# Kernel tuning notes

Measured on AMD Instinct MI355X. Metric: run time of the kernel, lower is better.

## Reference

```python
import math
import jax, jax.numpy as jnp
import numpy as np

B, T, D, H = 4, 1024, 1024, 8
HD = D // H  # head_dim = 128

def _trigram_dirs():
    # 8 trigrams = all sign combinations in {−1,+1}^3, L2-normalized (p=2, dim=1)
    t = np.array([[(i >> b & 1) * 2 - 1 for b in (2, 1, 0)] for i in range(8)], dtype=np.float32)
    return jnp.asarray(t / np.linalg.norm(t, axis=1, keepdims=True))

def setup_inputs() -> dict:
    key = jax.random.key(0)
    k1, k2, k3, k4 = jax.random.split(key, 4)
    x = jax.random.normal(k1, (B, T, D), dtype=jnp.float32)
    Wqkv = jax.random.normal(k2, (D, 3 * D), dtype=jnp.float32) * 0.02
    Wout = jax.random.normal(k3, (D, D), dtype=jnp.float32) * 0.02
    # head_scales init to 0 in the module; use nonzero values so the geo-bias path is exercised
    head_scales = jax.random.normal(k4, (H,), dtype=jnp.float32) * 0.1
    head_dirs = _trigram_dirs()  # [H, 3] buffer
    return {"x": x, "Wqkv": Wqkv, "Wout": Wout, "head_scales": head_scales, "head_dirs": head_dirs}

def reference(x, Wqkv, Wout, head_scales, head_dirs):
    b, t, d = x.shape
    scale = 1.0 / math.sqrt(HD)
    qkv = (x @ Wqkv).reshape(b, t, 3, H, HD)
    qkv = jnp.transpose(qkv, (2, 0, 3, 1, 4))  # [3, B, H, T, HD]
    q, k, v = qkv[0], qkv[1], qkv[2]
    # scores: [B, H, T, T]
    scores = jnp.einsum('bhqd,bhkd->bhqk', q, k) * scale
    # rank-1 trigram geometric bias from first 3 dims of q/k
    q_proj = jnp.einsum('bhtd,hd->bht', q[..., :3], head_dirs)
    k_proj = jnp.einsum('bhtd,hd->bht', k[..., :3], head_dirs)
    geo_bias = q_proj[..., :, None] * k_proj[..., None, :]  # [B, H, T, T]
    scores = scores + head_scales[None, :, None, None] * geo_bias
    causal = jnp.tril(jnp.ones((t, t), dtype=bool))
    scores = jnp.where(causal, scores, -jnp.inf)
    attn = jax.nn.softmax(scores, axis=-1)
    out = jnp.einsum('bhqk,bhkd->bhqd', attn, v)  # [B, H, T, HD]
    out = jnp.transpose(out, (0, 2, 1, 3)).reshape(b, t, d)
    return out @ Wout
```

## Files before the change

kernel.cpp:

```cpp
#include <hip/hip_runtime.h>
#include <stdint.h>

typedef __attribute__((ext_vector_type(8))) short short8;
typedef __attribute__((ext_vector_type(4))) short short4v;
typedef __attribute__((ext_vector_type(4))) float f32x4;

__device__ __forceinline__ short f2bf(float x) {
  union { float f; uint32_t u; } c; c.f = x;
  uint32_t r = (c.u + 0x7FFFu + ((c.u >> 16) & 1u)) >> 16;
  return (short)r;
}
__device__ __forceinline__ float b2f(short s) {
  union { uint32_t u; float f; } c; c.u = ((uint32_t)(uint16_t)s) << 16;
  return c.f;
}

__global__ __launch_bounds__(256) void cvt_kernel(const float* __restrict__ in,
                                                  short* __restrict__ out, int n4) {
  int i = blockIdx.x * 256 + threadIdx.x;
  const int stride = gridDim.x * 256;
  for (; i < n4; i += stride) {
    float4 v = reinterpret_cast<const float4*>(in)[i];
    short4v o;
    o.x = f2bf(v.x); o.y = f2bf(v.y); o.z = f2bf(v.z); o.w = f2bf(v.w);
    reinterpret_cast<short4v*>(out)[i] = o;
  }
}

__global__ __launch_bounds__(256) void tcvt_kernel(const float* __restrict__ in,
                                                   short* __restrict__ out, int K, int N) {
  __shared__ __align__(16) short tile[32][33];
  const int nb = blockIdx.x * 32, kb = blockIdx.y * 32;
  const int tx = threadIdx.x & 31, ty = threadIdx.x >> 5;
#pragma unroll
  for (int i = 0; i < 32; i += 8)
    tile[ty + i][tx] = f2bf(in[(size_t)(kb + ty + i) * N + nb + tx]);
  __syncthreads();
#pragma unroll
  for (int i = 0; i < 32; i += 8)
    out[(size_t)(nb + ty + i) * K + kb + tx] = tile[tx][ty + i];
}

__global__ __launch_bounds__(256) void vtrans_kernel(const short* __restrict__ qkvb,
                                                     short* __restrict__ vT) {
  __shared__ __align__(16) short tile[64][65];
  const int b = blockIdx.z;
  const int kv0 = blockIdx.x * 64, c0 = blockIdx.y * 64;
  const int tx = threadIdx.x & 15, ty = threadIdx.x >> 4;
  const short* src = qkvb + (size_t)(b * 1024) * 3072 + 2048;
#pragma unroll
  for (int i = 0; i < 64; i += 16) {
    int r = ty + i;
#pragma unroll
    for (int j = 0; j < 4; ++j)
      tile[r][tx * 4 + j] = src[(size_t)(kv0 + r) * 3072 + c0 + tx * 4 + j];
  }
  __syncthreads();
  short* dst = vT + (size_t)b * 1024 * 1024;
#pragma unroll
  for (int i = 0; i < 64; i += 16) {
    int cc = ty + i;
#pragma unroll
    for (int j = 0; j < 4; ++j)
      dst[(size_t)(c0 + cc) * 1024 + kv0 + tx * 4 + j] = tile[tx * 4 + j][cc];
  }
}

__global__ __launch_bounds__(256) void kproj_kernel(const short* __restrict__ qkvb,
                                                    const float* __restrict__ hdirs,
                                                    float* __restrict__ kproj) {
  const int i = blockIdx.x * 256 + threadIdx.x;
  const int bh = i >> 10, tt = i & 1023;
  const int b = bh >> 3, h = bh & 7;
  const float d0 = hdirs[h * 3], d1 = hdirs[h * 3 + 1], d2 = hdirs[h * 3 + 2];
  const short* kr = qkvb + (size_t)(b * 1024 + tt) * 3072 + 1024 + h * 128;
  kproj[i] = b2f(kr[0]) * d0 + b2f(kr[1]) * d1 + b2f(kr[2]) * d2;
}

template <int OUT_BF16>
__global__ __launch_bounds__(256) void gemm_kernel(const short* __restrict__ A,
                                                   const short* __restrict__ Bt,
                                                   void* __restrict__ Cout,
                                                   int K, int ldc) {
  __shared__ __align__(16) short Al[2][128 * 32];
  __shared__ __align__(16) short Bl[2][128 * 32];
  const int t = threadIdx.x;
  const int lane = t & 63, w = t >> 6;
  const int wr = w >> 1, wc = w & 1;
  const int g = lane >> 4, c16 = lane & 15;
  const int row0 = blockIdx.y * 128, col0 = blockIdx.x * 128;

  f32x4 acc[4][4];
#pragma unroll
  for (int m = 0; m < 4; ++m)
#pragma unroll
    for (int n = 0; n < 4; ++n) {
      f32x4 z = {0.0f, 0.0f, 0.0f, 0.0f};
      acc[m][n] = z;
    }

  auto stage = [&](int buf, int kt) {
    const int k0 = kt * 32;
#pragma unroll
    for (int i = 0; i < 2; ++i) {
      const int qb = i * 256 + (t & 192);
      const int q = qb + lane;
      const int r = q >> 2;
      const int c = (q & 3) ^ ((r >> 1) & 3);
      const short* ga = A + (size_t)(row0 + r) * K + k0 + c * 8;
      const short* gb = Bt + (size_t)(col0 + r) * K + k0 + c * 8;
      __builtin_amdgcn_global_load_lds((const __attribute__((address_space(1))) void*)ga,
                                       (__attribute__((address_space(3))) void*)&Al[buf][qb * 8],
                                       16, 0, 0);
      __builtin_amdgcn_global_load_lds((const __attribute__((address_space(1))) void*)gb,
                                       (__attribute__((address_space(3))) void*)&Bl[buf][qb * 8],
                                       16, 0, 0);
    }
  };

  stage(0, 0);
  __syncthreads();
  const int NK = K >> 5;
  int cur = 0;
  const int rA0 = wr * 64 + c16;
  const int rB0 = wc * 64 + c16;
  for (int kt = 0; kt < NK; ++kt) {
    if (kt + 1 < NK) stage(cur ^ 1, kt + 1);
    short8 aF[4], bF[4];
#pragma unroll
    for (int m = 0; m < 4; ++m) {
      const int r = rA0 + m * 16;
      const int c = g ^ ((r >> 1) & 3);
      aF[m] = *reinterpret_cast<const short8*>(&Al[cur][r * 32 + c * 8]);
    }
#pragma unroll
    for (int n = 0; n < 4; ++n) {
      const int r = rB0 + n * 16;
      const int c = g ^ ((r >> 1) & 3);
      bF[n] = *reinterpret_cast<const short8*>(&Bl[cur][r * 32 + c * 8]);
    }
#pragma unroll
    for (int m = 0; m < 4; ++m)
#pragma unroll
      for (int n = 0; n < 4; ++n)
        acc[m][n] = __builtin_amdgcn_mfma_f32_16x16x32_bf16(aF[m], bF[n], acc[m][n], 0, 0, 0);
    __syncthreads();
    cur ^= 1;
  }

  const int er = row0 + wr * 64 + g * 4;
  const int ec = col0 + wc * 64 + c16;
#pragma unroll
  for (int m = 0; m < 4; ++m)
#pragma unroll
    for (int n = 0; n < 4; ++n)
#pragma unroll
      for (int j = 0; j < 4; ++j) {
        const size_t off = (size_t)(er + m * 16 + j) * ldc + ec + n * 16;
        if (OUT_BF16)
          ((short*)Cout)[off] = f2bf(acc[m][n][j]);
        else
          ((float*)Cout)[off] = acc[m][n][j];
      }
}

__global__ __launch_bounds__(256) void attn_kernel(const short* __restrict__ qkvb,
                                                   const short* __restrict__ vT,
                                                   const float* __restrict__ head_scales,
                                                   const float* __restrict__ hdirs,
                                                   const float* __restrict__ kproj,
                                                   short* __restrict__ attnb) {
  __shared__ __align__(16) short Kl[2][64 * 128];
  __shared__ __align__(16) short Vl[2][128 * 64];
  __shared__ __align__(16) short P_lds[4][16 * 64];

  const int bid = blockIdx.x;
  const int bh = (bid & 7) * 4 + ((bid >> 3) & 3);
  const int qt = 15 - (bid >> 5);
  const int b = bh >> 3, h = bh & 7;
  const int t = threadIdx.x, lane = t & 63, w = t >> 6;
  const int g = lane >> 4, c16 = lane & 15;
  const int q0w = qt * 64 + w * 16;

  const short* qbase = qkvb + (size_t)(b * 1024) * 3072 + h * 128;
  const short* kbase = qbase + 1024;
  const short* vtb = vT + (size_t)bh * 128 * 1024;
  const float* kp = kproj + bh * 1024;

  const float hs = head_scales[h];
  const float d0 = hdirs[h * 3], d1 = hdirs[h * 3 + 1], d2 = hdirs[h * 3 + 2];
  const float scale = 0.08838834764831845f;

  short8 aQ[4];
  float hqp[4];
  {
    const short* qr = qbase + (size_t)(q0w + c16) * 3072 + g * 8;
#pragma unroll
    for (int kk = 0; kk < 4; ++kk) aQ[kk] = *reinterpret_cast<const short8*>(qr + kk * 32);
#pragma unroll
    for (int j = 0; j < 4; ++j) {
      const short* qa = qbase + (size_t)(q0w + g * 4 + j) * 3072;
      hqp[j] = hs * (b2f(qa[0]) * d0 + b2f(qa[1]) * d1 + b2f(qa[2]) * d2);
    }
  }

  float m_r[4], l_r[4];
  f32x4 accO[8];
#pragma unroll
  for (int j = 0; j < 4; ++j) { m_r[j] = -1e30f; l_r[j] = 0.0f; }
#pragma unroll
  for (int d = 0; d < 8; ++d) {
    f32x4 z = {0.0f, 0.0f, 0.0f, 0.0f};
    accO[d] = z;
  }

  short* Pw = P_lds[w];
  const short8 onesb = {(short)0x3F80, (short)0x3F80, (short)0x3F80, (short)0x3F80,
                        (short)0x3F80, (short)0x3F80, (short)0x3F80, (short)0x3F80};

  auto stageKV = [&](int buf, int kvt) {
    const int kv0 = kvt * 64;
#pragma unroll
    for (int i = 0; i < 4; ++i) {
      const int s = w * 4 + i;
      {
        const int r = s * 4 + g;
        const int c = c16 ^ (r & 7);
        const short* ga = kbase + (size_t)(kv0 + r) * 3072 + c * 8;
        __builtin_amdgcn_global_load_lds((const __attribute__((address_space(1))) void*)ga,
                                         (__attribute__((address_space(3))) void*)&Kl[buf][s * 512],
                                         16, 0, 0);
      }
      {
        const int r = s * 8 + (lane >> 3);
        const int c = (lane & 7) ^ (r & 7);
        const short* ga = vtb + (size_t)r * 1024 + kv0 + c * 8;
        __builtin_amdgcn_global_load_lds((const __attribute__((address_space(1))) void*)ga,
                                         (__attribute__((address_space(3))) void*)&Vl[buf][s * 512],
                                         16, 0, 0);
      }
    }
  };

  const int nkv = qt + 1;
  stageKV(0, 0);
  __syncthreads();
  int cur = 0;
  for (int kvt = 0; kvt < nkv; ++kvt) {
    const int kv0 = kvt * 64;
    if (kvt + 1 < nkv) stageKV(cur ^ 1, kvt + 1);
    const short* Kc = Kl[cur];
    const short* Vc = Vl[cur];

    float sc[4][4];
#pragma unroll
    for (int n = 0; n < 4; ++n) {
      f32x4 s4 = {0.0f, 0.0f, 0.0f, 0.0f};
      const int r = n * 16 + c16;
#pragma unroll
      for (int kk = 0; kk < 4; ++kk) {
        const int cch = (kk * 4 + g) ^ (r & 7);
        short8 bK = *reinterpret_cast<const short8*>(&Kc[r * 128 + cch * 8]);
        s4 = __builtin_amdgcn_mfma_f32_16x16x32_bf16(aQ[kk], bK, s4, 0, 0, 0);
      }
      const float kpv = kp[kv0 + r];
      const int ka = kv0 + r;
#pragma unroll
      for (int j = 0; j < 4; ++j) {
        const int qa = q0w + g * 4 + j;
        const float v = s4[j] * scale + hqp[j] * kpv;
        sc[n][j] = (ka <= qa) ? v : -1e30f;
      }
    }

    float mx[4];
#pragma unroll
    for (int j = 0; j < 4; ++j) {
      float v = fmaxf(fmaxf(sc[0][j], sc[1][j]), fmaxf(sc[2][j], sc[3][j]));
#pragma unroll
      for (int off = 8; off > 0; off >>= 1) v = fmaxf(v, __shfl_xor(v, off, 16));
      mx[j] = v;
    }
    const float dm = fmaxf(fmaxf(mx[0] - m_r[0], mx[1] - m_r[1]),
                           fmaxf(mx[2] - m_r[2], mx[3] - m_r[3]));
    if (__any(dm > 8.0f)) {
#pragma unroll
      for (int j = 0; j < 4; ++j) {
        const float mn = fmaxf(m_r[j], mx[j]);
        const float alpha = __expf(m_r[j] - mn);
        m_r[j] = mn;
        l_r[j] *= alpha;
#pragma unroll
        for (int d = 0; d < 8; ++d) accO[d][j] *= alpha;
      }
    }
#pragma unroll
    for (int n = 0; n < 4; ++n)
#pragma unroll
      for (int j = 0; j < 4; ++j) sc[n][j] = __expf(sc[n][j] - m_r[j]);

#pragma unroll
    for (int n = 0; n < 4; ++n) {
      const int col = n * 16 + c16;
      const int cb = col >> 3, o = col & 7;
#pragma unroll
      for (int j = 0; j < 4; ++j) {
        const int row = g * 4 + j;
        Pw[row * 64 + ((cb ^ (row & 7)) << 3) + o] = f2bf(sc[n][j]);
      }
    }
    short8 aP[2];
#pragma unroll
    for (int kk = 0; kk < 2; ++kk) {
      const int row = c16;
      const int cch = (kk * 4 + g) ^ (row & 7);
      aP[kk] = *reinterpret_cast<const short8*>(&Pw[row * 64 + cch * 8]);
    }

    f32x4 accS = {0.0f, 0.0f, 0.0f, 0.0f};
    accS = __builtin_amdgcn_mfma_f32_16x16x32_bf16(aP[0], onesb, accS, 0, 0, 0);
    accS = __builtin_amdgcn_mfma_f32_16x16x32_bf16(aP[1], onesb, accS, 0, 0, 0);
#pragma unroll
    for (int j = 0; j < 4; ++j) l_r[j] += accS[j];

#pragma unroll
    for (int dt = 0; dt < 8; ++dt) {
      const int r = dt * 16 + c16;
#pragma unroll
      for (int kk = 0; kk < 2; ++kk) {
        const int cch = (kk * 4 + g) ^ (r & 7);
        short8 bV = *reinterpret_cast<const short8*>(&Vc[r * 64 + cch * 8]);
        accO[dt] = __builtin_amdgcn_mfma_f32_16x16x32_bf16(aP[kk], bV, accO[dt], 0, 0, 0);
      }
    }
    __syncthreads();
    cur ^= 1;
  }

#pragma unroll
  for (int j = 0; j < 4; ++j) {
    const float inv = 1.0f / l_r[j];
    const size_t rowoff = (size_t)(b * 1024 + q0w + g * 4 + j) * 1024 + h * 128;
#pragma unroll
    for (int dt = 0; dt < 8; ++dt)
      attnb[rowoff + dt * 16 + c16] = f2bf(accO[dt][j] * inv);
  }
}

extern "C" void kernel_launch(void* const* d_in, const int* in_sizes, int n_in,
                              void* d_out, int out_size, void* d_ws, size_t ws_size,
                              hipStream_t stream) {
  const float* x = (const float*)d_in[0];
  const float* Wqkv = (const float*)d_in[1];
  const float* Wout = (const float*)d_in[2];
  const float* hscale = (const float*)d_in[3];
  const float* hdirs = (const float*)d_in[4];
  float* out = (float*)d_out;

  char* ws = (char*)d_ws;
  short* xb = (short*)(ws);
  short* wqkvT = (short*)(ws + (size_t)8 * 1024 * 1024);
  short* woutT = (short*)(ws + (size_t)14 * 1024 * 1024);
  short* qkvb = (short*)(ws + (size_t)16 * 1024 * 1024);
  short* vT = (short*)(ws + (size_t)40 * 1024 * 1024);
  short* attnb = (short*)(ws + (size_t)48 * 1024 * 1024);
  float* kproj = (float*)(ws);

  cvt_kernel<<<2048, 256, 0, stream>>>(x, xb, (4 * 1024 * 1024) / 4);
  tcvt_kernel<<<dim3(96, 32), 256, 0, stream>>>(Wqkv, wqkvT, 1024, 3072);
  tcvt_kernel<<<dim3(32, 32), 256, 0, stream>>>(Wout, woutT, 1024, 1024);
  gemm_kernel<1><<<dim3(24, 32), 256, 0, stream>>>(xb, wqkvT, (void*)qkvb, 1024, 3072);
  kproj_kernel<<<128, 256, 0, stream>>>(qkvb, hdirs, kproj);
  vtrans_kernel<<<dim3(16, 16, 4), 256, 0, stream>>>(qkvb, vT);
  attn_kernel<<<512, 256, 0, stream>>>(qkvb, vT, hscale, hdirs, kproj, attnb);
  gemm_kernel<0><<<dim3(8, 32), 256, 0, stream>>>(attnb, woutT, out, 1024, 1024);
}
```

Baseline: 118.6 us.

## Compute transposed QK^T so P stays in registers, dropping LDS round-trip

Swaps the MFMA operands so each lane holds scores for a single query row. The softmax max and sum then reduce with two cross-group shuffles, and the row sum no longer needs an MFMA against a ones vector. P is rebuilt into MFMA A-operand layout with register shuffles instead of an LDS write and read, and the k-projection values are staged through LDS. Softmax uses exp2 with log2e folded into the scale, which removes per-element multiplies, at the cost of extra shuffle instructions in the P repacking.

```diff
diff --git a/kernel.cpp b/kernel.cpp
--- a/kernel.cpp
+++ b/kernel.cpp
@@ -13,6 +13,9 @@
 __device__ __forceinline__ float b2f(short s) {
   union { uint32_t u; float f; } c; c.u = ((uint32_t)(uint16_t)s) << 16;
   return c.f;
+}
+__device__ __forceinline__ uint32_t pack2bf(float lo, float hi) {
+  return ((uint32_t)(uint16_t)f2bf(hi) << 16) | (uint32_t)(uint16_t)f2bf(lo);
 }
 
 __global__ __launch_bounds__(256) void cvt_kernel(const float* __restrict__ in,
@@ -172,7 +175,7 @@
                                                    short* __restrict__ attnb) {
   __shared__ __align__(16) short Kl[2][64 * 128];
   __shared__ __align__(16) short Vl[2][128 * 64];
-  __shared__ __align__(16) short P_lds[4][16 * 64];
+  __shared__ float kp_lds[2][64];
 
   const int bid = blockIdx.x;
   const int bh = (bid & 7) * 4 + ((bid >> 3) & 3);
@@ -181,42 +184,35 @@
   const int t = threadIdx.x, lane = t & 63, w = t >> 6;
   const int g = lane >> 4, c16 = lane & 15;
   const int q0w = qt * 64 + w * 16;
+  const int q_abs = q0w + c16;
 
   const short* qbase = qkvb + (size_t)(b * 1024) * 3072 + h * 128;
   const short* kbase = qbase + 1024;
   const short* vtb = vT + (size_t)bh * 128 * 1024;
   const float* kp = kproj + bh * 1024;
 
-  const float hs = head_scales[h];
-  const float d0 = hdirs[h * 3], d1 = hdirs[h * 3 + 1], d2 = hdirs[h * 3 + 2];
-  const float scale = 0.08838834764831845f;
+  const float LOG2E = 1.44269504088896f;
+  const float scale2 = 0.08838834764831845f * 1.44269504088896f;
 
   short8 aQ[4];
-  float hqp[4];
+  float hqp;
   {
-    const short* qr = qbase + (size_t)(q0w + c16) * 3072 + g * 8;
-#pragma unroll
-    for (int kk = 0; kk < 4; ++kk) aQ[kk] = *reinterpret_cast<const short8*>(qr + kk * 32);
-#pragma unroll
-    for (int j = 0; j < 4; ++j) {
-      const short* qa = qbase + (size_t)(q0w + g * 4 + j) * 3072;
-      hqp[j] = hs * (b2f(qa[0]) * d0 + b2f(qa[1]) * d1 + b2f(qa[2]) * d2);
-    }
-  }
-
-  float m_r[4], l_r[4];
+    const short* qr = qbase + (size_t)(q0w + c16) * 3072;
+#pragma unroll
+    for (int kk = 0; kk < 4; ++kk)
+      aQ[kk] = *reinterpret_cast<const short8*>(qr + kk * 32 + g * 8);
+    const float hs = head_scales[h];
+    hqp = hs * LOG2E *
+          (b2f(qr[0]) * hdirs[h * 3] + b2f(qr[1]) * hdirs[h * 3 + 1] + b2f(qr[2]) * hdirs[h * 3 + 2]);
+  }
+
+  float m_s = -1e30f, l_s = 0.0f;
   f32x4 accO[8];
-#pragma unroll
-  for (int j = 0; j < 4; ++j) { m_r[j] = -1e30f; l_r[j] = 0.0f; }
 #pragma unroll
   for (int d = 0; d < 8; ++d) {
     f32x4 z = {0.0f, 0.0f, 0.0f, 0.0f};
     accO[d] = z;
   }
-
-  short* Pw = P_lds[w];
-  const short8 onesb = {(short)0x3F80, (short)0x3F80, (short)0x3F80, (short)0x3F80,
-                        (short)0x3F80, (short)0x3F80, (short)0x3F80, (short)0x3F80};
 
   auto stageKV = [&](int buf, int kvt) {
     const int kv0 = kvt * 64;
@@ -240,6 +236,7 @@
                                          16, 0, 0);
       }
     }
+    if (lane < 16) kp_lds[buf][w * 16 + lane] = kp[kv0 + w * 16 + lane];
   };
 
   const int nkv = qt + 1;
@@ -251,8 +248,9 @@
     if (kvt + 1 < nkv) stageKV(cur ^ 1, kvt + 1);
     const short* Kc = Kl[cur];
     const short* Vc = Vl[cur];
-
-    float sc[4][4];
+    const float* kpc = kp_lds[cur];
+
+    float p[4][4];
 #pragma unroll
     for (int n = 0; n < 4; ++n) {
       f32x4 s4 = {0.0f, 0.0f, 0.0f, 0.0f};
@@ -261,67 +259,71 @@
       for (int kk = 0; kk < 4; ++kk) {
         const int cch = (kk * 4 + g) ^ (r & 7);
         short8 bK = *reinterpret_cast<const short8*>(&Kc[r * 128 + cch * 8]);
-        s4 = __builtin_amdgcn_mfma_f32_16x16x32_bf16(aQ[kk], bK, s4, 0, 0, 0);
-      }
-      const float kpv = kp[kv0 + r];
-      const int ka = kv0 + r;
+        s4 = __builtin_amdgcn_mfma_f32_16x16x32_bf16(bK, aQ[kk], s4, 0, 0, 0);
+      }
 #pragma unroll
       for (int j = 0; j < 4; ++j) {
-        const int qa = q0w + g * 4 + j;
-        const float v = s4[j] * scale + hqp[j] * kpv;
-        sc[n][j] = (ka <= qa) ? v : -1e30f;
-      }
-    }
-
-    float mx[4];
-#pragma unroll
-    for (int j = 0; j < 4; ++j) {
-      float v = fmaxf(fmaxf(sc[0][j], sc[1][j]), fmaxf(sc[2][j], sc[3][j]));
-#pragma unroll
-      for (int off = 8; off > 0; off >>= 1) v = fmaxf(v, __shfl_xor(v, off, 16));
-      mx[j] = v;
-    }
-    const float dm = fmaxf(fmaxf(mx[0] - m_r[0], mx[1] - m_r[1]),
-                           fmaxf(mx[2] - m_r[2], mx[3] - m_r[3]));
-    if (__any(dm > 8.0f)) {
-#pragma unroll
-      for (int j = 0; j < 4; ++j) {
-        const float mn = fmaxf(m_r[j], mx[j]);
-        const float alpha = __expf(m_r[j] - mn);
-        m_r[j] = mn;
-        l_r[j] *= alpha;
-#pragma unroll
-        for (int d = 0; d < 8; ++d) accO[d][j] *= alpha;
-      }
-    }
-#pragma unroll
-    for (int n = 0; n < 4; ++n)
-#pragma unroll
-      for (int j = 0; j < 4; ++j) sc[n][j] = __expf(sc[n][j] - m_r[j]);
-
-#pragma unroll
-    for (int n = 0; n < 4; ++n) {
-      const int col = n * 16 + c16;
-      const int cb = col >> 3, o = col & 7;
-#pragma unroll
-      for (int j = 0; j < 4; ++j) {
-        const int row = g * 4 + j;
-        Pw[row * 64 + ((cb ^ (row & 7)) << 3) + o] = f2bf(sc[n][j]);
-      }
-    }
-    short8 aP[2];
-#pragma unroll
-    for (int kk = 0; kk < 2; ++kk) {
-      const int row = c16;
-      const int cch = (kk * 4 + g) ^ (row & 7);
-      aP[kk] = *reinterpret_cast<const short8*>(&Pw[row * 64 + cch * 8]);
-    }
-
-    f32x4 accS = {0.0f, 0.0f, 0.0f, 0.0f};
-    accS = __builtin_amdgcn_mfma_f32_16x16x32_bf16(aP[0], onesb, accS, 0, 0, 0);
-    accS = __builtin_amdgcn_mfma_f32_16x16x32_bf16(aP[1], onesb, accS, 0, 0, 0);
-#pragma unroll
-    for (int j = 0; j < 4; ++j) l_r[j] += accS[j];
+        const int kloc = n * 16 + g * 4 + j;
+        const float v = s4[j] * scale2 + hqp * kpc[kloc];
+        p[n][j] = (kv0 + kloc <= q_abs) ? v : -1e30f;
+      }
+    }
+
+    float mx;
+    {
+      float a0 = fmaxf(fmaxf(p[0][0], p[0][1]), fmaxf(p[0][2], p[0][3]));
+      float a1 = fmaxf(fmaxf(p[1][0], p[1][1]), fmaxf(p[1][2], p[1][3]));
+      float a2 = fmaxf(fmaxf(p[2][0], p[2][1]), fmaxf(p[2][2], p[2][3]));
+      float a3 = fmaxf(fmaxf(p[3][0], p[3][1]), fmaxf(p[3][2], p[3][3]));
+      mx = fmaxf(fmaxf(a0, a1), fmaxf(a2, a3));
+      mx = fmaxf(mx, __shfl_xor(mx, 16, 64));
+      mx = fmaxf(mx, __shfl_xor(mx, 32, 64));
+    }
+
+    if (__any(mx - m_s > 11.54f)) {
+      const float mn = fmaxf(m_s, mx);
+      const float alpha = exp2f(m_s - mn);
+      m_s = mn;
+      l_s *= alpha;
+      float aO[4];
+#pragma unroll
+      for (int j = 0; j < 4; ++j) aO[j] = __shfl(alpha, g * 4 + j, 64);
+#pragma unroll
+      for (int d = 0; d < 8; ++d)
+#pragma unroll
+        for (int j = 0; j < 4; ++j) accO[d][j] *= aO[j];
+    }
+
+    float s01 = 0.0f, s23 = 0.0f;
+#pragma unroll
+    for (int n = 0; n < 4; ++n) {
+      float e0 = exp2f(p[n][0] - m_s), e1 = exp2f(p[n][1] - m_s);
+      float e2 = exp2f(p[n][2] - m_s), e3 = exp2f(p[n][3] - m_s);
+      p[n][0] = e0; p[n][1] = e1; p[n][2] = e2; p[n][3] = e3;
+      if (n < 2) s01 += (e0 + e1) + (e2 + e3); else s23 += (e0 + e1) + (e2 + e3);
+    }
+    float sum = s01 + s23;
+    sum += __shfl_xor(sum, 16, 64);
+    sum += __shfl_xor(sum, 32, 64);
+    l_s += sum;
+
+    uint32_t pk[4][2];
+#pragma unroll
+    for (int n = 0; n < 4; ++n) {
+      pk[n][0] = pack2bf(p[n][0], p[n][1]);
+      pk[n][1] = pack2bf(p[n][2], p[n][3]);
+    }
+
+    union { uint32_t d[4]; short8 s; } aPu[2];
+#pragma unroll
+    for (int kk = 0; kk < 2; ++kk)
+#pragma unroll
+      for (int wd = 0; wd < 4; ++wd) {
+        const int src = (2 * (g & 1) + (wd >> 1)) * 16 + c16;
+        const uint32_t v0 = (uint32_t)__shfl((int)pk[kk * 2][wd & 1], src, 64);
+        const uint32_t v1 = (uint32_t)__shfl((int)pk[kk * 2 + 1][wd & 1], src, 64);
+        aPu[kk].d[wd] = (g >= 2) ? v1 : v0;
+      }
 
 #pragma unroll
     for (int dt = 0; dt < 8; ++dt) {
@@ -330,20 +332,22 @@
       for (int kk = 0; kk < 2; ++kk) {
         const int cch = (kk * 4 + g) ^ (r & 7);
         short8 bV = *reinterpret_cast<const short8*>(&Vc[r * 64 + cch * 8]);
-        accO[dt] = __builtin_amdgcn_mfma_f32_16x16x32_bf16(aP[kk], bV, accO[dt], 0, 0, 0);
+        accO[dt] = __builtin_amdgcn_mfma_f32_16x16x32_bf16(aPu[kk].s, bV, accO[dt], 0, 0, 0);
       }
     }
     __syncthreads();
     cur ^= 1;
   }
 
+  float linv[4];
+#pragma unroll
+  for (int j = 0; j < 4; ++j) linv[j] = 1.0f / __shfl(l_s, g * 4 + j, 64);
 #pragma unroll
   for (int j = 0; j < 4; ++j) {
-    const float inv = 1.0f / l_r[j];
     const size_t rowoff = (size_t)(b * 1024 + q0w + g * 4 + j) * 1024 + h * 128;
 #pragma unroll
     for (int dt = 0; dt < 8; ++dt)
-      attnb[rowoff + dt * 16 + c16] = f2bf(accO[dt][j] * inv);
+      attnb[rowoff + dt * 16 + c16] = f2bf(accO[dt][j] * linv[j]);
   }
 }
 
```

New measurement: 120.6 us. Within noise of the previous version (+1.7%).
